# Performance work log

Hardware: AMD Instinct MI355X
Metric: run time of the kernel (lower is better)

Reference implementation:

```python
import jax, jax.numpy as jnp
import numpy as np

B, S, R, D, C = 32, 11, 16, 64, 512
NUM_ITER = 3
EPS = 1e-8
LN_EPS = 1e-3  # keras LayerNormalization default epsilon


def _grid():
    r = np.linspace(-1.0, 1.0, num=R)
    g = np.stack(np.meshgrid(r, r, indexing='ij'), axis=-1)  # [R,R,2]
    return jnp.asarray(g, dtype=jnp.float32)


def _ln(x, g, b):
    m = jnp.mean(x, -1, keepdims=True)
    v = jnp.mean((x - m) ** 2, -1, keepdims=True)
    return (x - m) * jax.lax.rsqrt(v + LN_EPS) * g + b


def setup_inputs() -> dict:
    key = jax.random.key(0)
    k = jax.random.split(key, 20)
    def W(i, shape, s=0.05):
        return jax.random.normal(k[i], shape, jnp.float32) * s
    return {
        'inputs': jax.random.normal(k[0], (B, R, R, C), jnp.float32),
        's_p0': jax.random.uniform(k[1], (B, S, 2), jnp.float32, -1.0, 1.0),
        's_s0': 0.1 + 0.01 * jax.random.normal(k[2], (B, S, 2), jnp.float32),
        'slots_mu': W(3, (1, S, D)),
        'es_w1': W(4, (2, 128)), 'es_b1': jnp.zeros((128,), jnp.float32),
        'es_w2': W(5, (128, C)), 'es_b2': jnp.zeros((C,), jnp.float32),
        'er_w': W(6, (2, D)), 'er_b': jnp.zeros((D,), jnp.float32),
        'pk_w': W(7, (C, D)), 'pk_b': jnp.zeros((D,), jnp.float32),
        'pv_w': W(8, (C, D)), 'pv_b': jnp.zeros((D,), jnp.float32),
        'pq_w': W(9, (D, D)), 'pq_b': jnp.zeros((D,), jnp.float32),
        'mi_w1': W(10, (D, 128)), 'mi_b1': jnp.zeros((128,), jnp.float32),
        'mi_w2': W(11, (128, D)), 'mi_b2': jnp.zeros((D,), jnp.float32),
        'ns_g': jnp.ones((D,), jnp.float32), 'ns_b': jnp.zeros((D,), jnp.float32),
        'nm_g': jnp.ones((D,), jnp.float32), 'nm_b': jnp.zeros((D,), jnp.float32),
        'gru_k': W(12, (D, 3 * D)), 'gru_rk': W(13, (D, 3 * D)),
        'gru_b': jnp.zeros((2, 3 * D), jnp.float32),
        'mlp_w1': W(14, (D, 128)), 'mlp_b1': jnp.zeros((128,), jnp.float32),
        'mlp_w2': W(15, (128, D)), 'mlp_b2': jnp.zeros((D,), jnp.float32),
    }


def reference(inputs, s_p0, s_s0, slots_mu, es_w1, es_b1, es_w2, es_b2,
              er_w, er_b, pk_w, pk_b, pv_w, pv_b, pq_w, pq_b,
              mi_w1, mi_b1, mi_w2, mi_b2, ns_g, ns_b, nm_g, nm_b,
              gru_k, gru_rk, gru_b, mlp_w1, mlp_b1, mlp_w2, mlp_b2):
    N = R * R
    grid = _grid()                 # [R,R,2]
    gflat = grid.reshape(N, 2)     # [N,2]

    # SoftPositionEmbed_start: pos embedding and inputs are identical across the
    # slot axis, so compute once per batch element then broadcast later.
    pos = jnp.maximum(grid @ es_w1 + es_b1, 0.0) @ es_w2 + es_b2  # [R,R,C]
    x = (inputs + pos).reshape(B, N, C)                            # [B,N,C]
    inputs_k = x @ pk_w + pk_b                                     # [B,N,D]
    inputs_v = x @ pv_w + pv_b                                     # [B,N,D]

    def ff(t):  # mlp_inputs: Dense(128, relu) -> Dense(64)
        return jnp.maximum(t @ mi_w1 + mi_b1, 0.0) @ mi_w2 + mi_b2

    def gru(u, h):  # keras GRUCell (reset_after=True, default)
        xz, xr, xh = jnp.split(u @ gru_k + gru_b[0], 3, axis=-1)
        hz, hr, hh = jnp.split(h @ gru_rk + gru_b[1], 3, axis=-1)
        z = jax.nn.sigmoid(xz + hz)
        r = jax.nn.sigmoid(xr + hr)
        hcand = jnp.tanh(xh + r * hh)
        return z * h + (1.0 - z) * hcand

    slots = jnp.broadcast_to(slots_mu, (B, S, D))
    s_p, s_s = s_p0, s_s0
    attn = None
    for ind in range(NUM_ITER + 1):
        # SoftPositionEmbed_rel: per-slot relative grid encoding
        rel = (gflat[None, None] - s_p[:, :, None, :]) / s_s[:, :, None, :]  # [B,S,N,2]
        pe = rel @ er_w + er_b                                               # [B,S,N,D]
        k = ff(inputs_k[:, None] + pe)                                       # [B,S,N,D]
        v = ff(inputs_v[:, None] + pe)                                       # [B,S,N,D]
        slots_prev = slots
        q = (_ln(slots, ns_g, ns_b) @ pq_w + pq_b) * (D ** -0.5)             # [B,S,D]
        logits = jnp.einsum('bsnd,bsd->bns', k, q)                           # [B,N,S]
        attn = jax.nn.softmax(logits, axis=-1) + EPS                         # softmax over slots
        attn = attn / jnp.sum(attn, axis=1, keepdims=True)                   # renorm over inputs
        updates = jnp.einsum('bns,bsnd->bsd', attn, v)                       # [B,S,D]

        # calcSP -- the double reshape matches the original TF code exactly
        a = attn.transpose(0, 2, 1).reshape(B, R, R, S).reshape(B, S, R, R)
        aw = a[..., None]                                                    # [B,S,R,R,1]
        wp = jnp.sum(grid[None, None] * aw, axis=(2, 3))                     # [B,S,2]
        d2 = (grid[None, None] - wp[:, :, None, None, :]) ** 2
        ws = jnp.sqrt(jnp.sum(d2 * (aw + 1e-11), axis=(2, 3)))               # [B,S,2]
        s_p = wp
        s_s = jnp.clip(ws, 0.001, 5.0)

        if ind < NUM_ITER:
            slots = gru(updates, slots_prev)
            slots = slots + (jnp.maximum(_ln(slots, nm_g, nm_b) @ mlp_w1 + mlp_b1, 0.0) @ mlp_w2 + mlp_b2)
    return slots, s_p, s_s, attn
```

## Files before the change

### kernel.cpp

```cpp
#include <hip/hip_runtime.h>
#include <cmath>

#define B 32
#define S 11
#define R 16
#define D 64
#define C 512
#define N 256
#define LN_EPS 1e-3f

typedef unsigned short u16;
typedef unsigned int   u32;

using bf16x8 = __attribute__((ext_vector_type(8))) short;
using f32x4  = __attribute__((ext_vector_type(4))) float;

__device__ __forceinline__ float grid_coord(int i) {
    return -1.0f + (2.0f / 15.0f) * (float)i;
}

__device__ __forceinline__ u16 f2bf(float x) {
    union { float f; u32 u; } c; c.f = x;
    u32 r = c.u + 0x7fffu + ((c.u >> 16) & 1u);
    return (u16)(r >> 16);
}

__device__ __forceinline__ float bf2f(u16 h) {
    union { u32 u; float f; } c; c.u = ((u32)h) << 16; return c.f;
}

__global__ __launch_bounds__(256) void pre1_kernel(
    const float* __restrict__ es_w1, const float* __restrict__ es_b1,
    const float* __restrict__ es_w2, const float* __restrict__ es_b2,
    const float* __restrict__ mi_w1, const float* __restrict__ mi_b1,
    const float* __restrict__ pk_w, const float* __restrict__ pk_b,
    const float* __restrict__ pv_w, const float* __restrict__ pv_b,
    const float* __restrict__ er_w, const float* __restrict__ er_b,
    const float* __restrict__ slots_mu, const float* __restrict__ s_p0,
    const float* __restrict__ s_s0,
    float* __restrict__ pos,
    u16* __restrict__ wkT, u16* __restrict__ wvT,
    float* __restrict__ ewp,
    float* __restrict__ slots0, float* __restrict__ sp0, float* __restrict__ ss0) {
    int bid = blockIdx.x;
    int t = threadIdx.x;
    if (bid < 256) {
        int n = bid;
        float g0 = grid_coord(n >> 4), g1 = grid_coord(n & 15);
        __shared__ float h[128];
        if (t < 128) {
            float hj = es_b1[t] + g0 * es_w1[t] + g1 * es_w1[128 + t];
            h[t] = fmaxf(hj, 0.0f);
        }
        __syncthreads();
        #pragma unroll
        for (int c0 = 0; c0 < C; c0 += 256) {
            int c = c0 + t;
            float acc = es_b2[c];
            #pragma unroll 16
            for (int jj = 0; jj < 128; ++jj) acc += h[jj] * es_w2[jj * C + c];
            pos[n * C + c] = acc;
        }
    } else if (bid < 770) {
        int idx = (bid - 256) * 256 + t;
        if (idx < 131072) {
            int mat = idx >> 16;
            int i = idx & 65535;
            int c = i >> 7, j = i & 127;
            const float* pw = mat ? pv_w : pk_w;
            float acc = 0.f;
            #pragma unroll 8
            for (int k = 0; k < 64; ++k) acc += pw[c * 64 + k] * mi_w1[k * 128 + j];
            u16* dst = mat ? wvT : wkT;
            dst[j * 512 + c] = f2bf(acc);
        } else if (idx < 131584) {
            int i = idx - 131072;
            int tt = i >> 7, j = i & 127;
            float acc = 0.f;
            if (tt == 0) {
                for (int k = 0; k < 64; ++k) acc += er_w[k] * mi_w1[k * 128 + j];
            } else if (tt == 1) {
                for (int k = 0; k < 64; ++k) acc += er_w[64 + k] * mi_w1[k * 128 + j];
            } else if (tt == 2) {
                for (int k = 0; k < 64; ++k) acc += (pk_b[k] + er_b[k]) * mi_w1[k * 128 + j];
                acc += mi_b1[j];
            } else {
                for (int k = 0; k < 64; ++k) acc += (pv_b[k] + er_b[k]) * mi_w1[k * 128 + j];
                acc += mi_b1[j];
            }
            ewp[i] = acc;
        }
    } else {
        int idx = (bid - 770) * 256 + t;
        slots0[idx] = slots_mu[idx % (S * D)];
        if (idx < B * S * 2) { sp0[idx] = s_p0[idx]; ss0[idx] = s_s0[idx]; }
    }
}

__global__ __launch_bounds__(256) void pre2_kernel(
    const float* __restrict__ inputs, const float* __restrict__ pos,
    const u16* __restrict__ wkT,
    const float* __restrict__ ewp,
    const float* __restrict__ slots0,
    const float* __restrict__ ns_g, const float* __restrict__ ns_b,
    const float* __restrict__ pq_w, const float* __restrict__ pq_b,
    const float* __restrict__ mi_w2, const float* __restrict__ mi_b2,
    float* __restrict__ GkT, u16* __restrict__ Gv16,
    float* __restrict__ w2q, float* __restrict__ b2q) {
    int bid = blockIdx.x;
    int t = threadIdx.x;
    if (bid < 512) {
        int row0 = bid * 16;
        __shared__ u16 Xs[16 * 512];
        __shared__ float bbk2[128], bbv2[128];
        if (t < 128) { bbk2[t] = ewp[256 + t]; bbv2[t] = ewp[384 + t]; }
        const float4* in4 = (const float4*)(inputs + (size_t)row0 * C);
        #pragma unroll
        for (int it = 0; it < 8; ++it) {
            int f = it * 256 + t;
            int lr = f >> 7;
            int c = (f & 127) * 4;
            float4 a = in4[f];
            float4 p = *(const float4*)(pos + (size_t)((row0 + lr) & (N - 1)) * C + c);
            u32 lo = (u32)f2bf(a.x + p.x) | ((u32)f2bf(a.y + p.y) << 16);
            u32 hi = (u32)f2bf(a.z + p.z) | ((u32)f2bf(a.w + p.w) << 16);
            int cs = c ^ ((lr & 7) << 3);
            *(uint2*)&Xs[lr * 512 + cs] = make_uint2(lo, hi);
        }
        __syncthreads();

        int w = t >> 6, l = t & 63;
        int l16 = l & 15, lq = l >> 4;
        int wc = w * 32;
        int b = row0 >> 8, nb = row0 & (N - 1);

        f32x4 acc[2][2];
        #pragma unroll
        for (int m = 0; m < 2; ++m)
            #pragma unroll
            for (int nt = 0; nt < 2; ++nt) acc[m][nt] = (f32x4){0.f, 0.f, 0.f, 0.f};

        for (int kt = 0; kt < 16; ++kt) {
            int k0 = kt * 32 + lq * 8;
            int ks = k0 ^ ((l16 & 7) << 3);
            bf16x8 xf = *(const bf16x8*)&Xs[l16 * 512 + ks];
            #pragma unroll
            for (int m = 0; m < 2; ++m) {
                const u16* Wm = wkT + (size_t)m * 65536;
                #pragma unroll
                for (int nt = 0; nt < 2; ++nt) {
                    bf16x8 wf = *(const bf16x8*)(Wm + (size_t)(wc + nt * 16 + l16) * 512 + k0);
                    acc[m][nt] = __builtin_amdgcn_mfma_f32_16x16x32_bf16(xf, wf, acc[m][nt], 0, 0, 0);
                }
            }
        }
        #pragma unroll
        for (int nt = 0; nt < 2; ++nt) {
            #pragma unroll
            for (int r = 0; r < 4; ++r) {
                int j = wc + nt * 16 + l16;
                int n2 = nb + lq * 4 + r;
                GkT[((size_t)b * 128 + j) * 256 + n2] = acc[0][nt][r] + bbk2[j];
                Gv16[((size_t)b * 256 + n2) * 128 + j] = f2bf(acc[1][nt][r] + bbv2[j]);
            }
        }
    } else {
        int bs = bid - 512;
        __shared__ float xlds[64], qs[64];
        if (t < 64) {
            float x = slots0[bs * D + t];
            float sum = x;
            #pragma unroll
            for (int off = 32; off > 0; off >>= 1) sum += __shfl_xor(sum, off);
            float m = sum * (1.0f / 64.0f);
            float dx = x - m;
            float vs = dx * dx;
            #pragma unroll
            for (int off = 32; off > 0; off >>= 1) vs += __shfl_xor(vs, off);
            float var = vs * (1.0f / 64.0f);
            xlds[t] = dx * rsqrtf(var + LN_EPS) * ns_g[t] + ns_b[t];
        }
        __syncthreads();
        if (t < 64) {
            float acc = pq_b[t];
            #pragma unroll 8
            for (int i = 0; i < 64; ++i) acc += xlds[i] * pq_w[i * D + t];
            qs[t] = acc * 0.125f;
        }
        __syncthreads();
        if (t < 128) {
            float sacc = 0.f;
            #pragma unroll 8
            for (int dd = 0; dd < 64; ++dd) sacc += mi_w2[t * 64 + dd] * qs[dd];
            w2q[bs * 128 + t] = sacc;
        }
        if (t < 64) {
            float v = mi_b2[t] * qs[t];
            #pragma unroll
            for (int off = 32; off > 0; off >>= 1) v += __shfl_xor(v, off);
            if (t == 0) b2q[bs] = v;
        }
    }
}

__global__ __launch_bounds__(256) void kv0_kernel(
    const float* __restrict__ GkT, const float* __restrict__ ewp,
    const float* __restrict__ sp0, const float* __restrict__ ss0,
    const float* __restrict__ w2q, const float* __restrict__ b2q,
    float* __restrict__ logits) {
    int orig = blockIdx.x;
    int u = (orig & 7) * 88 + (orig >> 3);
    int half = u & 1, bs = u >> 1;
    int b = bs / S, s = bs - b * S;
    int t = threadIdx.x;
    __shared__ float e0s[128], e1s[128], wqs[128], lgp[128], rl0[128], rl1[128];
    if (t < 128) {
        e0s[t] = ewp[t]; e1s[t] = ewp[128 + t];
        wqs[t] = w2q[bs * 128 + t];
        float p0 = sp0[bs * 2 + 0], p1 = sp0[bs * 2 + 1];
        float q0 = ss0[bs * 2 + 0], q1 = ss0[bs * 2 + 1];
        int n = half * 128 + t;
        rl0[t] = (grid_coord(n >> 4) - p0) / q0;
        rl1[t] = (grid_coord(n & 15) - p1) / q1;
    }
    __syncthreads();
    int n_loc = t & 127, jh = t >> 7;
    float r0 = rl0[n_loc], r1 = rl1[n_loc];
    const float* Gb = GkT + ((size_t)b * 128 + jh * 64) * 256 + half * 128 + n_loc;
    float acc = 0.f;
    #pragma unroll 8
    for (int j = 0; j < 64; ++j) {
        int jj = jh * 64 + j;
        float h = Gb[(size_t)j * 256] + r0 * e0s[jj] + r1 * e1s[jj];
        acc += fmaxf(h, 0.f) * wqs[jj];
    }
    if (jh) lgp[n_loc] = acc;
    __syncthreads();
    if (!jh)
        logits[((size_t)b * S + s) * N + half * 128 + n_loc] = acc + lgp[n_loc] + b2q[bs];
}

__global__ __launch_bounds__(256) void upkv_kernel(
    int ind,
    const float* __restrict__ lgts_r, float* __restrict__ lgts_w,
    const float* __restrict__ sp_r, const float* __restrict__ ss_r,
    float* __restrict__ sp_w, float* __restrict__ ss_w,
    const float* __restrict__ slots_r, float* __restrict__ slots_w,
    const float* __restrict__ GkT, const u16* __restrict__ Gv16,
    const float* __restrict__ ewp,
    const float* __restrict__ gru_k, const float* __restrict__ gru_rk,
    const float* __restrict__ gru_b,
    const float* __restrict__ nm_g, const float* __restrict__ nm_b,
    const float* __restrict__ mlp_w1, const float* __restrict__ mlp_b1,
    const float* __restrict__ mlp_w2, const float* __restrict__ mlp_b2,
    const float* __restrict__ ns_g, const float* __restrict__ ns_b,
    const float* __restrict__ pq_w, const float* __restrict__ pq_b,
    const float* __restrict__ mi_w2, const float* __restrict__ mi_b2,
    float* __restrict__ out_slots) {
    int orig = blockIdx.x;
    int u = (orig & 7) * 88 + (orig >> 3);
    int half = u & 1, bs = u >> 1;
    int b = bs / S, s = bs - b * S;
    int t = threadIdx.x;
    int wv = t >> 6, l = t & 63, d = l;

    __shared__ float e0s[128], e1s[128], wqs[128], lgp[128];
    __shared__ float rlo0[256], rlo1[256], rn0[128], rn1[128];
    __shared__ float a_l[256], aH2[256], ul[64], hl[64], gx[192], gh[192];
    __shared__ float xl[64], snl[64], hb[128], xq[64], qs[64], red[12], sc[4];

    if (t < 128) { e0s[t] = ewp[t]; e1s[t] = ewp[128 + t]; }
    {
        float p0 = sp_r[bs * 2 + 0], p1 = sp_r[bs * 2 + 1];
        float q0 = ss_r[bs * 2 + 0], q1 = ss_r[bs * 2 + 1];
        rlo0[t] = (grid_coord(t >> 4) - p0) / q0;
        rlo1[t] = (grid_coord(t & 15) - p1) / q1;
    }

    float m = -1e30f, lg[S];
    #pragma unroll
    for (int ss2 = 0; ss2 < S; ++ss2) {
        lg[ss2] = lgts_r[((size_t)b * S + ss2) * N + t];
        m = fmaxf(m, lg[ss2]);
    }
    float sum = 0.f, e_own = 0.f;
    #pragma unroll
    for (int ss2 = 0; ss2 < S; ++ss2) {
        float e = expf(lg[ss2] - m);
        sum += e;
        if (ss2 == s) e_own = e;
    }
    float a_n = e_own / sum + 1e-8f;
    float g0 = grid_coord(t >> 4), g1 = grid_coord(t & 15);
    {
        float sa = a_n, s0 = a_n * g0, s1 = a_n * g1;
        #pragma unroll
        for (int off = 32; off > 0; off >>= 1) {
            sa += __shfl_xor(sa, off);
            s0 += __shfl_xor(s0, off);
            s1 += __shfl_xor(s1, off);
        }
        if (l == 0) { red[wv] = sa; red[4 + wv] = s0; red[8 + wv] = s1; }
    }
    __syncthreads();
    float SA = red[0] + red[1] + red[2] + red[3];
    float wp0 = (red[4] + red[5] + red[6] + red[7]) / SA;
    float wp1 = (red[8] + red[9] + red[10] + red[11]) / SA;
    float inv_sa = 1.0f / SA;
    __syncthreads();
    {
        float av = a_n * inv_sa + 1e-11f;
        float d0 = g0 - wp0, d1 = g1 - wp1;
        float t0 = d0 * d0 * av, t1 = d1 * d1 * av;
        #pragma unroll
        for (int off = 32; off > 0; off >>= 1) {
            t0 += __shfl_xor(t0, off);
            t1 += __shfl_xor(t1, off);
        }
        if (l == 0) { red[wv] = t0; red[4 + wv] = t1; }
        a_l[t] = a_n * inv_sa;
    }
    __syncthreads();
    float T0c = fminf(fmaxf(sqrtf(red[0] + red[1] + red[2] + red[3]), 0.001f), 5.0f);
    float T1c = fminf(fmaxf(sqrtf(red[4] + red[5] + red[6] + red[7]), 0.001f), 5.0f);

    {
        int j = t & 127, nh = t >> 7;
        const u16* Gr = Gv16 + ((size_t)b * 256 + nh * 128) * 128 + j;
        float e0j = e0s[j], e1j = e1s[j];
        float acc = 0.f;
        #pragma unroll 8
        for (int i = 0; i < 128; ++i) {
            int n = nh * 128 + i;
            float h = bf2f(Gr[(size_t)i * 128]) + rlo0[n] * e0j + rlo1[n] * e1j;
            acc += a_l[n] * fmaxf(h, 0.f);
        }
        aH2[t] = acc;
    }
    __syncthreads();
    if (t < 64) {
        float u2 = mi_b2[d];
        #pragma unroll 8
        for (int j = 0; j < 128; ++j)
            u2 += (aH2[j] + aH2[128 + j]) * mi_w2[j * 64 + d];
        ul[d] = u2;
        hl[d] = slots_r[bs * D + d];
    }
    __syncthreads();
    if (t < 192) {
        float ax = gru_b[t], ah = gru_b[192 + t];
        #pragma unroll 8
        for (int i = 0; i < 64; ++i) {
            ax += ul[i] * gru_k[i * 192 + t];
            ah += hl[i] * gru_rk[i * 192 + t];
        }
        gx[t] = ax; gh[t] = ah;
    }
    __syncthreads();
    if (t < 64) {
        float z = 1.f / (1.f + expf(-(gx[d] + gh[d])));
        float r = 1.f / (1.f + expf(-(gx[64 + d] + gh[64 + d])));
        float hc = tanhf(gx[128 + d] + r * gh[128 + d]);
        float sn = z * hl[d] + (1.f - z) * hc;
        snl[d] = sn;
        float sm = sn;
        #pragma unroll
        for (int off = 32; off > 0; off >>= 1) sm += __shfl_xor(sm, off);
        float mm = sm * (1.0f / 64.0f);
        float dx = sn - mm;
        float vs = dx * dx;
        #pragma unroll
        for (int off = 32; off > 0; off >>= 1) vs += __shfl_xor(vs, off);
        float var = vs * (1.0f / 64.0f);
        xl[d] = dx * rsqrtf(var + LN_EPS) * nm_g[d] + nm_b[d];
    }
    __syncthreads();
    if (t < 128) {
        float h1 = mlp_b1[t];
        #pragma unroll 8
        for (int i = 0; i < 64; ++i) h1 += xl[i] * mlp_w1[i * 128 + t];
        hb[t] = fmaxf(h1, 0.f);
    }
    __syncthreads();
    if (t < 64) {
        float o = mlp_b2[d];
        #pragma unroll 8
        for (int j = 0; j < 128; ++j) o += hb[j] * mlp_w2[j * D + d];
        float res = snl[d] + o;
        slots_w[bs * D + d] = res;
        if (ind == 2) out_slots[bs * D + d] = res;
        float sm = res;
        #pragma unroll
        for (int off = 32; off > 0; off >>= 1) sm += __shfl_xor(sm, off);
        float mm = sm * (1.0f / 64.0f);
        float dx = res - mm;
        float vs = dx * dx;
        #pragma unroll
        for (int off = 32; off > 0; off >>= 1) vs += __shfl_xor(vs, off);
        float var = vs * (1.0f / 64.0f);
        xq[d] = dx * rsqrtf(var + LN_EPS) * ns_g[d] + ns_b[d];
    }
    __syncthreads();
    if (t < 64) {
        float acc = pq_b[d];
        #pragma unroll 8
        for (int i = 0; i < 64; ++i) acc += xq[i] * pq_w[i * D + d];
        qs[d] = acc * 0.125f;
    }
    __syncthreads();
    {
        float wql = 0.f;
        if (t < 128) {
            #pragma unroll 8
            for (int dd = 0; dd < 64; ++dd) wql += mi_w2[t * 64 + dd] * qs[dd];
        }
        float b2v = 0.f;
        if (t < 64) {
            b2v = mi_b2[d] * qs[d];
            #pragma unroll
            for (int off = 32; off > 0; off >>= 1) b2v += __shfl_xor(b2v, off);
        }
        if (t < 128) wqs[t] = wql;
        if (t == 0) {
            sc[0] = b2v;
            sp_w[bs * 2 + 0] = wp0; sp_w[bs * 2 + 1] = wp1;
            ss_w[bs * 2 + 0] = T0c; ss_w[bs * 2 + 1] = T1c;
        }
        if (t < 128) {
            int n = half * 128 + t;
            rn0[t] = (grid_coord(n >> 4) - wp0) / T0c;
            rn1[t] = (grid_coord(n & 15) - wp1) / T1c;
        }
    }
    __syncthreads();

    {
        int n_loc = t & 127, jh = t >> 7;
        float r0 = rn0[n_loc], r1 = rn1[n_loc];
        const float* Gb = GkT + ((size_t)b * 128 + jh * 64) * 256 + half * 128 + n_loc;
        float acc = 0.f;
        #pragma unroll 8
        for (int j = 0; j < 64; ++j) {
            int jj = jh * 64 + j;
            float h = Gb[(size_t)j * 256] + r0 * e0s[jj] + r1 * e1s[jj];
            acc += fmaxf(h, 0.f) * wqs[jj];
        }
        if (jh) lgp[n_loc] = acc;
        __syncthreads();
        if (!jh)
            lgts_w[((size_t)b * S + s) * N + half * 128 + n_loc] = acc + lgp[n_loc] + sc[0];
    }
}

__global__ __launch_bounds__(256) void fin_kernel(
    const float* __restrict__ lgts_r,
    float* __restrict__ attn_out, float* __restrict__ osp, float* __restrict__ oss) {
    int orig = blockIdx.x;
    int bs = (orig & 7) * 44 + (orig >> 3);
    int b = bs / S, s = bs - b * S;
    int t = threadIdx.x;
    int wv = t >> 6, l = t & 63;
    __shared__ float red[12];
    float m = -1e30f, lg[S];
    #pragma unroll
    for (int ss2 = 0; ss2 < S; ++ss2) {
        lg[ss2] = lgts_r[((size_t)b * S + ss2) * N + t];
        m = fmaxf(m, lg[ss2]);
    }
    float sum = 0.f, e_own = 0.f;
    #pragma unroll
    for (int ss2 = 0; ss2 < S; ++ss2) {
        float e = expf(lg[ss2] - m);
        sum += e;
        if (ss2 == s) e_own = e;
    }
    float a_n = e_own / sum + 1e-8f;
    float g0 = grid_coord(t >> 4), g1 = grid_coord(t & 15);
    float sa = a_n, s0 = a_n * g0, s1 = a_n * g1;
    #pragma unroll
    for (int off = 32; off > 0; off >>= 1) {
        sa += __shfl_xor(sa, off);
        s0 += __shfl_xor(s0, off);
        s1 += __shfl_xor(s1, off);
    }
    if (l == 0) { red[wv] = sa; red[4 + wv] = s0; red[8 + wv] = s1; }
    __syncthreads();
    float SA = red[0] + red[1] + red[2] + red[3];
    float wp0 = (red[4] + red[5] + red[6] + red[7]) / SA;
    float wp1 = (red[8] + red[9] + red[10] + red[11]) / SA;
    float inv_sa = 1.0f / SA;
    float av = a_n * inv_sa + 1e-11f;
    float d0 = g0 - wp0, d1 = g1 - wp1;
    float t0 = d0 * d0 * av, t1 = d1 * d1 * av;
    #pragma unroll
    for (int off = 32; off > 0; off >>= 1) {
        t0 += __shfl_xor(t0, off);
        t1 += __shfl_xor(t1, off);
    }
    __syncthreads();
    if (l == 0) { red[wv] = t0; red[4 + wv] = t1; }
    __syncthreads();
    if (t == 0) {
        osp[bs * 2 + 0] = wp0;
        osp[bs * 2 + 1] = wp1;
        oss[bs * 2 + 0] = fminf(fmaxf(sqrtf(red[0] + red[1] + red[2] + red[3]), 0.001f), 5.0f);
        oss[bs * 2 + 1] = fminf(fmaxf(sqrtf(red[4] + red[5] + red[6] + red[7]), 0.001f), 5.0f);
    }
    attn_out[((size_t)b * N + t) * S + s] = a_n * inv_sa;
}

extern "C" void kernel_launch(void* const* d_in, const int* in_sizes, int n_in,
                              void* d_out, int out_size, void* d_ws, size_t ws_size,
                              hipStream_t stream) {
    const float* inputs  = (const float*)d_in[0];
    const float* s_p0    = (const float*)d_in[1];
    const float* s_s0    = (const float*)d_in[2];
    const float* slots_mu= (const float*)d_in[3];
    const float* es_w1   = (const float*)d_in[4];
    const float* es_b1   = (const float*)d_in[5];
    const float* es_w2   = (const float*)d_in[6];
    const float* es_b2   = (const float*)d_in[7];
    const float* er_w    = (const float*)d_in[8];
    const float* er_b    = (const float*)d_in[9];
    const float* pk_w    = (const float*)d_in[10];
    const float* pk_b    = (const float*)d_in[11];
    const float* pv_w    = (const float*)d_in[12];
    const float* pv_b    = (const float*)d_in[13];
    const float* pq_w    = (const float*)d_in[14];
    const float* pq_b    = (const float*)d_in[15];
    const float* mi_w1   = (const float*)d_in[16];
    const float* mi_b1   = (const float*)d_in[17];
    const float* mi_w2   = (const float*)d_in[18];
    const float* mi_b2   = (const float*)d_in[19];
    const float* ns_g    = (const float*)d_in[20];
    const float* ns_b    = (const float*)d_in[21];
    const float* nm_g    = (const float*)d_in[22];
    const float* nm_b    = (const float*)d_in[23];
    const float* gru_k   = (const float*)d_in[24];
    const float* gru_rk  = (const float*)d_in[25];
    const float* gru_b   = (const float*)d_in[26];
    const float* mlp_w1  = (const float*)d_in[27];
    const float* mlp_b1  = (const float*)d_in[28];
    const float* mlp_w2  = (const float*)d_in[29];
    const float* mlp_b2  = (const float*)d_in[30];

    float* ws     = (float*)d_ws;
    float* pos    = ws;
    float* GkT    = pos    + 131072;
    u16*   Gv16   = (u16*)(GkT + 1048576);
    float* lgts0  = GkT + 2097152;
    float* lgts1  = lgts0  + 90112;
    float* slots0 = lgts1  + 90112;
    float* slots1 = slots0 + 22528;
    float* sp0    = slots1 + 22528;
    float* ss0    = sp0    + 704;
    float* sp1    = ss0    + 704;
    float* ss1    = sp1    + 704;
    float* w2qb   = ss1    + 704;
    float* b2qb   = w2qb   + 45056;
    float* ewp    = b2qb   + 352;
    u16*   wkT    = (u16*)(ewp + 512);
    u16*   wvT    = wkT + 65536;

    float* out      = (float*)d_out;
    float* out_sp   = out + B * S * D;
    float* out_ss   = out_sp + B * S * 2;
    float* attn_out = out_ss + B * S * 2;

    pre1_kernel<<<858, 256, 0, stream>>>(es_w1, es_b1, es_w2, es_b2,
                                         mi_w1, mi_b1,
                                         pk_w, pk_b, pv_w, pv_b, er_w, er_b,
                                         slots_mu, s_p0, s_s0,
                                         pos, wkT, wvT, ewp, slots0, sp0, ss0);
    pre2_kernel<<<864, 256, 0, stream>>>(inputs, pos, wkT, ewp, slots0,
                                         ns_g, ns_b, pq_w, pq_b, mi_w2, mi_b2,
                                         GkT, Gv16, w2qb, b2qb);
    kv0_kernel<<<704, 256, 0, stream>>>(GkT, ewp, sp0, ss0, w2qb, b2qb, lgts0);
    upkv_kernel<<<704, 256, 0, stream>>>(0, lgts0, lgts1, sp0, ss0, sp1, ss1,
                                         slots0, slots1, GkT, Gv16, ewp,
                                         gru_k, gru_rk, gru_b, nm_g, nm_b,
                                         mlp_w1, mlp_b1, mlp_w2, mlp_b2,
                                         ns_g, ns_b, pq_w, pq_b, mi_w2, mi_b2, out);
    upkv_kernel<<<704, 256, 0, stream>>>(1, lgts1, lgts0, sp1, ss1, sp0, ss0,
                                         slots1, slots0, GkT, Gv16, ewp,
                                         gru_k, gru_rk, gru_b, nm_g, nm_b,
                                         mlp_w1, mlp_b1, mlp_w2, mlp_b2,
                                         ns_g, ns_b, pq_w, pq_b, mi_w2, mi_b2, out);
    upkv_kernel<<<704, 256, 0, stream>>>(2, lgts0, lgts1, sp0, ss0, sp1, ss1,
                                         slots0, slots1, GkT, Gv16, ewp,
                                         gru_k, gru_rk, gru_b, nm_g, nm_b,
                                         mlp_w1, mlp_b1, mlp_w2, mlp_b2,
                                         ns_g, ns_b, pq_w, pq_b, mi_w2, mi_b2, out);
    fin_kernel<<<352, 256, 0, stream>>>(lgts1, attn_out, out_sp, out_ss);
}
```

Measured before the change: 120.3 us.

## Fuse initial logits computation into projection GEMM kernel and dedupe per-slot query prep

Removes the separate kv0 kernel by computing the first-iteration logits inside pre2 from the just-computed Gk tile held in shared memory. It also exploits that the initial slots are identical across the batch, so w2q and b2q are computed once per slot (11 blocks in pre1) instead of once per batch×slot. This saves a kernel launch, a global re-read of GkT, and redundant query work. In exchange, pre2 uses more shared memory and only 176 of its 256 threads do the logit loop.

```diff
diff --git a/kernel.cpp b/kernel.cpp
--- a/kernel.cpp
+++ b/kernel.cpp
@@ -33,15 +33,19 @@
     const float* __restrict__ es_w1, const float* __restrict__ es_b1,
     const float* __restrict__ es_w2, const float* __restrict__ es_b2,
     const float* __restrict__ mi_w1, const float* __restrict__ mi_b1,
+    const float* __restrict__ mi_w2, const float* __restrict__ mi_b2,
     const float* __restrict__ pk_w, const float* __restrict__ pk_b,
     const float* __restrict__ pv_w, const float* __restrict__ pv_b,
     const float* __restrict__ er_w, const float* __restrict__ er_b,
     const float* __restrict__ slots_mu, const float* __restrict__ s_p0,
     const float* __restrict__ s_s0,
+    const float* __restrict__ ns_g, const float* __restrict__ ns_b,
+    const float* __restrict__ pq_w, const float* __restrict__ pq_b,
     float* __restrict__ pos,
     u16* __restrict__ wkT, u16* __restrict__ wvT,
     float* __restrict__ ewp,
-    float* __restrict__ slots0, float* __restrict__ sp0, float* __restrict__ ss0) {
+    float* __restrict__ slots0, float* __restrict__ sp0, float* __restrict__ ss0,
+    float* __restrict__ w2q0, float* __restrict__ b2q0) {
     int bid = blockIdx.x;
     int t = threadIdx.x;
     if (bid < 256) {
@@ -73,7 +77,7 @@
             for (int k = 0; k < 64; ++k) acc += pw[c * 64 + k] * mi_w1[k * 128 + j];
             u16* dst = mat ? wvT : wkT;
             dst[j * 512 + c] = f2bf(acc);
-        } else if (idx < 131584) {
+        } else {
             int i = idx - 131072;
             int tt = i >> 7, j = i & 127;
             float acc = 0.f;
@@ -90,85 +94,15 @@
             }
             ewp[i] = acc;
         }
-    } else {
+    } else if (bid < 858) {
         int idx = (bid - 770) * 256 + t;
         slots0[idx] = slots_mu[idx % (S * D)];
         if (idx < B * S * 2) { sp0[idx] = s_p0[idx]; ss0[idx] = s_s0[idx]; }
-    }
-}
-
-__global__ __launch_bounds__(256) void pre2_kernel(
-    const float* __restrict__ inputs, const float* __restrict__ pos,
-    const u16* __restrict__ wkT,
-    const float* __restrict__ ewp,
-    const float* __restrict__ slots0,
-    const float* __restrict__ ns_g, const float* __restrict__ ns_b,
-    const float* __restrict__ pq_w, const float* __restrict__ pq_b,
-    const float* __restrict__ mi_w2, const float* __restrict__ mi_b2,
-    float* __restrict__ GkT, u16* __restrict__ Gv16,
-    float* __restrict__ w2q, float* __restrict__ b2q) {
-    int bid = blockIdx.x;
-    int t = threadIdx.x;
-    if (bid < 512) {
-        int row0 = bid * 16;
-        __shared__ u16 Xs[16 * 512];
-        __shared__ float bbk2[128], bbv2[128];
-        if (t < 128) { bbk2[t] = ewp[256 + t]; bbv2[t] = ewp[384 + t]; }
-        const float4* in4 = (const float4*)(inputs + (size_t)row0 * C);
-        #pragma unroll
-        for (int it = 0; it < 8; ++it) {
-            int f = it * 256 + t;
-            int lr = f >> 7;
-            int c = (f & 127) * 4;
-            float4 a = in4[f];
-            float4 p = *(const float4*)(pos + (size_t)((row0 + lr) & (N - 1)) * C + c);
-            u32 lo = (u32)f2bf(a.x + p.x) | ((u32)f2bf(a.y + p.y) << 16);
-            u32 hi = (u32)f2bf(a.z + p.z) | ((u32)f2bf(a.w + p.w) << 16);
-            int cs = c ^ ((lr & 7) << 3);
-            *(uint2*)&Xs[lr * 512 + cs] = make_uint2(lo, hi);
-        }
-        __syncthreads();
-
-        int w = t >> 6, l = t & 63;
-        int l16 = l & 15, lq = l >> 4;
-        int wc = w * 32;
-        int b = row0 >> 8, nb = row0 & (N - 1);
-
-        f32x4 acc[2][2];
-        #pragma unroll
-        for (int m = 0; m < 2; ++m)
-            #pragma unroll
-            for (int nt = 0; nt < 2; ++nt) acc[m][nt] = (f32x4){0.f, 0.f, 0.f, 0.f};
-
-        for (int kt = 0; kt < 16; ++kt) {
-            int k0 = kt * 32 + lq * 8;
-            int ks = k0 ^ ((l16 & 7) << 3);
-            bf16x8 xf = *(const bf16x8*)&Xs[l16 * 512 + ks];
-            #pragma unroll
-            for (int m = 0; m < 2; ++m) {
-                const u16* Wm = wkT + (size_t)m * 65536;
-                #pragma unroll
-                for (int nt = 0; nt < 2; ++nt) {
-                    bf16x8 wf = *(const bf16x8*)(Wm + (size_t)(wc + nt * 16 + l16) * 512 + k0);
-                    acc[m][nt] = __builtin_amdgcn_mfma_f32_16x16x32_bf16(xf, wf, acc[m][nt], 0, 0, 0);
-                }
-            }
-        }
-        #pragma unroll
-        for (int nt = 0; nt < 2; ++nt) {
-            #pragma unroll
-            for (int r = 0; r < 4; ++r) {
-                int j = wc + nt * 16 + l16;
-                int n2 = nb + lq * 4 + r;
-                GkT[((size_t)b * 128 + j) * 256 + n2] = acc[0][nt][r] + bbk2[j];
-                Gv16[((size_t)b * 256 + n2) * 128 + j] = f2bf(acc[1][nt][r] + bbv2[j]);
-            }
-        }
     } else {
-        int bs = bid - 512;
-        __shared__ float xlds[64], qs[64];
+        int s = bid - 858;
+        __shared__ float xlds[64], qs2[64];
         if (t < 64) {
-            float x = slots0[bs * D + t];
+            float x = slots_mu[s * D + t];
             float sum = x;
             #pragma unroll
             for (int off = 32; off > 0; off >>= 1) sum += __shfl_xor(sum, off);
@@ -185,59 +119,117 @@
             float acc = pq_b[t];
             #pragma unroll 8
             for (int i = 0; i < 64; ++i) acc += xlds[i] * pq_w[i * D + t];
-            qs[t] = acc * 0.125f;
+            qs2[t] = acc * 0.125f;
         }
         __syncthreads();
         if (t < 128) {
             float sacc = 0.f;
             #pragma unroll 8
-            for (int dd = 0; dd < 64; ++dd) sacc += mi_w2[t * 64 + dd] * qs[dd];
-            w2q[bs * 128 + t] = sacc;
+            for (int dd = 0; dd < 64; ++dd) sacc += mi_w2[t * 64 + dd] * qs2[dd];
+            w2q0[s * 128 + t] = sacc;
         }
         if (t < 64) {
-            float v = mi_b2[t] * qs[t];
+            float v = mi_b2[t] * qs2[t];
             #pragma unroll
             for (int off = 32; off > 0; off >>= 1) v += __shfl_xor(v, off);
-            if (t == 0) b2q[bs] = v;
-        }
-    }
-}
-
-__global__ __launch_bounds__(256) void kv0_kernel(
-    const float* __restrict__ GkT, const float* __restrict__ ewp,
-    const float* __restrict__ sp0, const float* __restrict__ ss0,
-    const float* __restrict__ w2q, const float* __restrict__ b2q,
-    float* __restrict__ logits) {
-    int orig = blockIdx.x;
-    int u = (orig & 7) * 88 + (orig >> 3);
-    int half = u & 1, bs = u >> 1;
-    int b = bs / S, s = bs - b * S;
+            if (t == 0) b2q0[s] = v;
+        }
+    }
+}
+
+__global__ __launch_bounds__(256) void pre2_kernel(
+    const float* __restrict__ inputs, const float* __restrict__ pos,
+    const u16* __restrict__ wkT,
+    const float* __restrict__ ewp,
+    const float* __restrict__ s_p0, const float* __restrict__ s_s0,
+    const float* __restrict__ w2q0, const float* __restrict__ b2q0,
+    float* __restrict__ GkT, u16* __restrict__ Gv16,
+    float* __restrict__ lgts0) {
+    int bid = blockIdx.x;
     int t = threadIdx.x;
-    __shared__ float e0s[128], e1s[128], wqs[128], lgp[128], rl0[128], rl1[128];
+    int row0 = bid * 16;
+    __shared__ u16 Xs[16 * 512];
+    __shared__ float Gs[16 * 129];
+    __shared__ float w2qs[11 * 132];
+    __shared__ float e0s[128], e1s[128], bbk2[128], bbv2[128];
     if (t < 128) {
         e0s[t] = ewp[t]; e1s[t] = ewp[128 + t];
-        wqs[t] = w2q[bs * 128 + t];
-        float p0 = sp0[bs * 2 + 0], p1 = sp0[bs * 2 + 1];
-        float q0 = ss0[bs * 2 + 0], q1 = ss0[bs * 2 + 1];
-        int n = half * 128 + t;
-        rl0[t] = (grid_coord(n >> 4) - p0) / q0;
-        rl1[t] = (grid_coord(n & 15) - p1) / q1;
-    }
-    __syncthreads();
-    int n_loc = t & 127, jh = t >> 7;
-    float r0 = rl0[n_loc], r1 = rl1[n_loc];
-    const float* Gb = GkT + ((size_t)b * 128 + jh * 64) * 256 + half * 128 + n_loc;
-    float acc = 0.f;
-    #pragma unroll 8
-    for (int j = 0; j < 64; ++j) {
-        int jj = jh * 64 + j;
-        float h = Gb[(size_t)j * 256] + r0 * e0s[jj] + r1 * e1s[jj];
-        acc += fmaxf(h, 0.f) * wqs[jj];
-    }
-    if (jh) lgp[n_loc] = acc;
-    __syncthreads();
-    if (!jh)
-        logits[((size_t)b * S + s) * N + half * 128 + n_loc] = acc + lgp[n_loc] + b2q[bs];
+        bbk2[t] = ewp[256 + t]; bbv2[t] = ewp[384 + t];
+    }
+    for (int i = t; i < 11 * 128; i += 256)
+        w2qs[(i >> 7) * 132 + (i & 127)] = w2q0[i];
+
+    const float4* in4 = (const float4*)(inputs + (size_t)row0 * C);
+    #pragma unroll
+    for (int it = 0; it < 8; ++it) {
+        int f = it * 256 + t;
+        int lr = f >> 7;
+        int c = (f & 127) * 4;
+        float4 a = in4[f];
+        float4 p = *(const float4*)(pos + (size_t)((row0 + lr) & (N - 1)) * C + c);
+        u32 lo = (u32)f2bf(a.x + p.x) | ((u32)f2bf(a.y + p.y) << 16);
+        u32 hi = (u32)f2bf(a.z + p.z) | ((u32)f2bf(a.w + p.w) << 16);
+        int cs = c ^ ((lr & 7) << 3);
+        *(uint2*)&Xs[lr * 512 + cs] = make_uint2(lo, hi);
+    }
+    __syncthreads();
+
+    int w = t >> 6, l = t & 63;
+    int l16 = l & 15, lq = l >> 4;
+    int wc = w * 32;
+    int b = row0 >> 8, nb = row0 & (N - 1);
+
+    f32x4 acc[2][2];
+    #pragma unroll
+    for (int m = 0; m < 2; ++m)
+        #pragma unroll
+        for (int nt = 0; nt < 2; ++nt) acc[m][nt] = (f32x4){0.f, 0.f, 0.f, 0.f};
+
+    for (int kt = 0; kt < 16; ++kt) {
+        int k0 = kt * 32 + lq * 8;
+        int ks = k0 ^ ((l16 & 7) << 3);
+        bf16x8 xf = *(const bf16x8*)&Xs[l16 * 512 + ks];
+        #pragma unroll
+        for (int m = 0; m < 2; ++m) {
+            const u16* Wm = wkT + (size_t)m * 65536;
+            #pragma unroll
+            for (int nt = 0; nt < 2; ++nt) {
+                bf16x8 wf = *(const bf16x8*)(Wm + (size_t)(wc + nt * 16 + l16) * 512 + k0);
+                acc[m][nt] = __builtin_amdgcn_mfma_f32_16x16x32_bf16(xf, wf, acc[m][nt], 0, 0, 0);
+            }
+        }
+    }
+    #pragma unroll
+    for (int nt = 0; nt < 2; ++nt) {
+        #pragma unroll
+        for (int r = 0; r < 4; ++r) {
+            int j = wc + nt * 16 + l16;
+            int nl = lq * 4 + r;
+            int n2 = nb + nl;
+            float gk = acc[0][nt][r] + bbk2[j];
+            GkT[((size_t)b * 128 + j) * 256 + n2] = gk;
+            Gs[nl * 129 + j] = gk;
+            Gv16[((size_t)b * 256 + n2) * 128 + j] = f2bf(acc[1][nt][r] + bbv2[j]);
+        }
+    }
+    __syncthreads();
+
+    if (t < 176) {
+        int nl = t & 15, s = t >> 4;
+        int n = nb + nl;
+        int i2 = (b * S + s) * 2;
+        float p0 = s_p0[i2 + 0], p1 = s_p0[i2 + 1];
+        float q0 = s_s0[i2 + 0], q1 = s_s0[i2 + 1];
+        float r0 = (grid_coord(n >> 4) - p0) / q0;
+        float r1 = (grid_coord(n & 15) - p1) / q1;
+        float accl = 0.f;
+        #pragma unroll 8
+        for (int j = 0; j < 128; ++j) {
+            float h = Gs[nl * 129 + j] + r0 * e0s[j] + r1 * e1s[j];
+            accl += fmaxf(h, 0.f) * w2qs[s * 132 + j];
+        }
+        lgts0[((size_t)b * S + s) * N + n] = accl + b2q0[s];
+    }
 }
 
 __global__ __launch_bounds__(256) void upkv_kernel(
@@ -556,9 +548,9 @@
     float* ss0    = sp0    + 704;
     float* sp1    = ss0    + 704;
     float* ss1    = sp1    + 704;
-    float* w2qb   = ss1    + 704;
-    float* b2qb   = w2qb   + 45056;
-    float* ewp    = b2qb   + 352;
+    float* w2q0   = ss1    + 704;
+    float* b2q0   = w2q0   + 1408;
+    float* ewp    = b2q0   + 16;
     u16*   wkT    = (u16*)(ewp + 512);
     u16*   wvT    = wkT + 65536;
 
@@ -567,15 +559,16 @@
     float* out_ss   = out_sp + B * S * 2;
     float* attn_out = out_ss + B * S * 2;
 
-    pre1_kernel<<<858, 256, 0, stream>>>(es_w1, es_b1, es_w2, es_b2,
-                                         mi_w1, mi_b1,
+    pre1_kernel<<<869, 256, 0, stream>>>(es_w1, es_b1, es_w2, es_b2,
+                                         mi_w1, mi_b1, mi_w2, mi_b2,
                                          pk_w, pk_b, pv_w, pv_b, er_w, er_b,
                                          slots_mu, s_p0, s_s0,
-                                         pos, wkT, wvT, ewp, slots0, sp0, ss0);
-    pre2_kernel<<<864, 256, 0, stream>>>(inputs, pos, wkT, ewp, slots0,
-                                         ns_g, ns_b, pq_w, pq_b, mi_w2, mi_b2,
-                                         GkT, Gv16, w2qb, b2qb);
-    kv0_kernel<<<704, 256, 0, stream>>>(GkT, ewp, sp0, ss0, w2qb, b2qb, lgts0);
+                                         ns_g, ns_b, pq_w, pq_b,
+                                         pos, wkT, wvT, ewp,
+                                         slots0, sp0, ss0, w2q0, b2q0);
+    pre2_kernel<<<512, 256, 0, stream>>>(inputs, pos, wkT, ewp,
+                                         s_p0, s_s0, w2q0, b2q0,
+                                         GkT, Gv16, lgts0);
     upkv_kernel<<<704, 256, 0, stream>>>(0, lgts0, lgts1, sp0, ss0, sp1, ss1,
                                          slots0, slots1, GkT, Gv16, ewp,
                                          gru_k, gru_rk, gru_b, nm_g, nm_b,
```

New measurement: 120.3 us. Within noise of the previous version (+0.0%).
